# Performance work log

Measured on AMD Instinct MI355X. Metric: run time of the kernel, lower is better.

## Reference

```python
import jax, jax.numpy as jnp
import numpy as np

N_NODES = 50000
N_EDGES = 800000
N_GRAPHS = 500
NEG_SLOPE = 0.2
BN_EPS = 1e-5


def gat_layer(x, src, dst, W, al, ar, b):
    # x: [N, F_in]; W: [F_in, H*D]; al/ar: [H, D]; b: [H*D]
    H, D = al.shape
    feat = (x @ W).reshape(N_NODES, H, D)          # [N,H,D]
    el = jnp.sum(feat * al, axis=-1)               # [N,H] src-side score
    er = jnp.sum(feat * ar, axis=-1)               # [N,H] dst-side score
    e = el[src] + er[dst]                          # [E,H]
    e = jnp.where(e > 0, e, NEG_SLOPE * e)         # leaky_relu(0.2)
    # edge softmax over incoming edges of each dst node
    m = jax.ops.segment_max(e, dst, num_segments=N_NODES)       # [N,H]
    ex = jnp.exp(e - m[dst])                                    # [E,H]
    denom = jax.ops.segment_sum(ex, dst, num_segments=N_NODES)  # [N,H]
    alpha = ex / denom[dst]                                     # [E,H]
    # weighted scatter-aggregation of source features
    msg = feat[src] * alpha[:, :, None]                          # [E,H,D]
    out = jax.ops.segment_sum(msg, dst, num_segments=N_NODES)    # [N,H,D]
    return out + b.reshape(H, D)


def batch_norm(x, gamma, beta):
    # training-mode BN over node dimension (biased variance, as torch)
    mu = jnp.mean(x, axis=0)
    var = jnp.mean((x - mu) ** 2, axis=0)
    return gamma * (x - mu) * jax.lax.rsqrt(var + BN_EPS) + beta


def setup_inputs() -> dict:
    key = jax.random.key(0)
    ks = jax.random.split(key, 20)
    s = lambda shape, k, scale=0.05: jax.random.normal(ks[k], shape, jnp.float32) * scale
    return {
        "x": jax.random.normal(ks[0], (N_NODES, 128), jnp.float32),
        "edge_src": jax.random.randint(ks[1], (N_EDGES,), 0, N_NODES),
        "edge_dst": jax.random.randint(ks[2], (N_EDGES,), 0, N_NODES),
        "graph_ids": jax.random.randint(ks[3], (N_NODES,), 0, N_GRAPHS),
        "W0": s((128, 128), 4), "al0": s((4, 32), 5), "ar0": s((4, 32), 6), "b0": jnp.zeros((128,), jnp.float32),
        "W1": s((128, 128), 7), "al1": s((4, 32), 8), "ar1": s((4, 32), 9), "b1": jnp.zeros((128,), jnp.float32),
        "W2": s((128, 32), 10), "al2": s((1, 32), 11), "ar2": s((1, 32), 12), "b2": jnp.zeros((32,), jnp.float32),
        "g0": jnp.ones((128,), jnp.float32), "beta0": jnp.zeros((128,), jnp.float32),
        "g1": jnp.ones((128,), jnp.float32), "beta1": jnp.zeros((128,), jnp.float32),
        "Wc": s((32, 10), 13), "bc": jnp.zeros((10,), jnp.float32),
    }


def reference(x, edge_src, edge_dst, graph_ids,
              W0, al0, ar0, b0, W1, al1, ar1, b1, W2, al2, ar2, b2,
              g0, beta0, g1, beta1, Wc, bc):
    # layer 0: GAT -> flatten heads -> BN -> ReLU (dropout = identity in eval)
    h = gat_layer(x, edge_src, edge_dst, W0, al0, ar0, b0).reshape(N_NODES, -1)
    h = jax.nn.relu(batch_norm(h, g0, beta0))
    # layer 1
    h = gat_layer(h, edge_src, edge_dst, W1, al1, ar1, b1).reshape(N_NODES, -1)
    h = jax.nn.relu(batch_norm(h, g1, beta1))
    # layer 2 (single head) -> squeeze head dim
    h = gat_layer(h, edge_src, edge_dst, W2, al2, ar2, b2)[:, 0, :]  # [N, 32]
    # sum pooling per graph
    hg = jax.ops.segment_sum(h, graph_ids, num_segments=N_GRAPHS)    # [G, 32]
    return hg @ Wc + bc                                              # [G, 10]
```

## Files before the change

kernel.cpp:

```cpp
#include <hip/hip_runtime.h>
#include <math.h>

#define NNODES 50000
#define NEDGES 800000
#define NGRAPHS 500
#define NEG_SLOPE 0.2f
#define BN_EPS 1e-5f
#define NRANGE 196
#define RH_EPB 4096
#define RH_NB ((NEDGES + RH_EPB - 1) / RH_EPB)
#define MAXRE 5120
#define BN_NB 200
#define BN_RPB 250

typedef unsigned int uint;
typedef unsigned short ushort;
typedef __attribute__((ext_vector_type(8))) short bf16x8;
typedef __attribute__((ext_vector_type(4))) float f32x4;

__device__ __forceinline__ float bf2f(ushort u) { return __uint_as_float(((uint)u) << 16); }
__device__ __forceinline__ float bflo(uint u)   { return __uint_as_float(u << 16); }
__device__ __forceinline__ float bfhi(uint u)   { return __uint_as_float(u & 0xffff0000u); }
__device__ __forceinline__ ushort f2bf(float f) {
    uint u = __float_as_uint(f);
    u = (u + 0x7fffu + ((u >> 16) & 1u)) >> 16;
    return (ushort)u;
}

__global__ __launch_bounds__(256) void prep_hist_kernel(
        const float* __restrict__ W0, const float* __restrict__ W1,
        const float* __restrict__ W2, ushort* __restrict__ Wt0,
        ushort* __restrict__ Wt1, ushort* __restrict__ Wt2,
        const int* __restrict__ dst, int* __restrict__ rhist) {
    int t = blockIdx.x * 256 + threadIdx.x;
    if (t < 16384) {
        int k = t >> 7, m = t & 127;
        Wt0[m * 128 + k] = f2bf(W0[t]);
    } else if (t < 32768) {
        int i = t - 16384;
        int k = i >> 7, m = i & 127;
        Wt1[m * 128 + k] = f2bf(W1[i]);
    } else if (t < 36864) {
        int i = t - 32768;
        int k = i >> 5, m = i & 31;
        Wt2[m * 128 + k] = f2bf(W2[i]);
    }
    __shared__ int cnt[NRANGE];
    for (int i = threadIdx.x; i < NRANGE; i += 256) cnt[i] = 0;
    __syncthreads();
    int base = blockIdx.x * RH_EPB;
    int end = base + RH_EPB; if (end > NEDGES) end = NEDGES;
    for (int i = base + threadIdx.x; i < end; i += 256) atomicAdd(&cnt[dst[i] >> 8], 1);
    __syncthreads();
    for (int i = threadIdx.x; i < NRANGE; i += 256)
        if (cnt[i]) atomicAdd(&rhist[i], cnt[i]);
}

__global__ void range_scan_kernel(const int* __restrict__ rhist, int* __restrict__ rbase,
                                  int* __restrict__ rcursor, int* __restrict__ rowptr) {
    __shared__ int ls[256];
    int t = threadIdx.x;
    ls[t] = (t < NRANGE) ? rhist[t] : 0;
    __syncthreads();
    for (int off = 1; off < 256; off <<= 1) {
        int u = (t >= off) ? ls[t - off] : 0;
        __syncthreads();
        ls[t] += u;
        __syncthreads();
    }
    if (t < NRANGE) {
        int b = (t == 0) ? 0 : ls[t - 1];
        rbase[t] = b;
        rcursor[t] = b;
    }
    if (t == 0) { rbase[NRANGE] = NEDGES; rowptr[NNODES] = NEDGES; }
}

__global__ void reorder_kernel(const int* __restrict__ src, const int* __restrict__ dst,
                               int* __restrict__ rcursor, uint* __restrict__ bucket) {
    __shared__ int cnt[NRANGE];
    __shared__ int bofs[NRANGE];
    for (int i = threadIdx.x; i < NRANGE; i += 256) cnt[i] = 0;
    __syncthreads();
    int base = blockIdx.x * RH_EPB;
    int end = base + RH_EPB; if (end > NEDGES) end = NEDGES;
    for (int i = base + threadIdx.x; i < end; i += 256) atomicAdd(&cnt[dst[i] >> 8], 1);
    __syncthreads();
    for (int i = threadIdx.x; i < NRANGE; i += 256) {
        int c = cnt[i];
        bofs[i] = c ? atomicAdd(&rcursor[i], c) : 0;
    }
    __syncthreads();
    for (int i = threadIdx.x; i < NRANGE; i += 256) cnt[i] = 0;
    __syncthreads();
    for (int i = base + threadIdx.x; i < end; i += 256) {
        int d = dst[i], r = d >> 8;
        int loc = atomicAdd(&cnt[r], 1);
        bucket[bofs[r] + loc] = (uint)src[i] | ((uint)(d & 255) << 16);
    }
}

__global__ __launch_bounds__(256) void range_csr_kernel(const int* __restrict__ rbase,
                                                        const uint* __restrict__ bucket,
                                                        int* __restrict__ rowptr,
                                                        int* __restrict__ csr_src) {
    __shared__ uint ebuf[MAXRE];
    __shared__ int deg[256], excl[256], cur[256];
    const int r = blockIdx.x;
    const int b0 = rbase[r];
    const int cnt = rbase[r + 1] - b0;
    const int t = threadIdx.x;
    deg[t] = 0; cur[t] = 0;
    __syncthreads();
    for (int i = t; i < cnt; i += 256) {
        uint e = bucket[b0 + i];
        ebuf[i] = e;
        atomicAdd(&deg[e >> 16], 1);
    }
    __syncthreads();
    excl[t] = deg[t];
    __syncthreads();
    for (int off = 1; off < 256; off <<= 1) {
        int u = (t >= off) ? excl[t - off] : 0;
        __syncthreads();
        excl[t] += u;
        __syncthreads();
    }
    int myExcl = (t == 0) ? 0 : excl[t - 1];
    __syncthreads();
    excl[t] = myExcl;
    __syncthreads();
    int node = r * 256 + t;
    if (node < NNODES) rowptr[node] = b0 + myExcl;
    for (int i = t; i < cnt; i += 256) {
        uint e = ebuf[i];
        int dl = e >> 16;
        int loc = atomicAdd(&cur[dl], 1);
        csr_src[b0 + excl[dl] + loc] = (int)(e & 0xffffu);
    }
}

template <int M, bool HASBN>
__global__ __launch_bounds__(256) void gemm_mfma_kernel(
        const void* __restrict__ Xv, const ushort* __restrict__ Wt,
        const float* __restrict__ scale, const float* __restrict__ shift,
        const float* __restrict__ al, const float* __restrict__ ar,
        ushort* __restrict__ Y, float* __restrict__ el, float* __restrict__ er, int N) {
    constexpr int H   = M / 32;
    constexpr int BR  = (M == 128) ? 64 : 128;
    constexpr int RT  = (M == 128) ? 4 : 2;
    constexpr int CT  = 2;
    constexpr int LDK = 136;
    __shared__ ushort xs[BR][LDK];
    __shared__ ushort ws[M][LDK];
    __shared__ float scs[128], shs[128];

    const int tid = threadIdx.x, wv = tid >> 6, lane = tid & 63;
    const int rowBase = blockIdx.x * BR;

    if (HASBN) {
        if (tid < 128) {
            scs[tid] = scale[tid];
            shs[tid] = shift[tid];
        }
        __syncthreads();
    }

    if (HASBN) {
        const ushort* X = (const ushort*)Xv;
        for (int i = tid; i < BR * 16; i += 256) {
            int rr = i >> 4, q = i & 15;
            int gr = rowBase + rr;
            uint4 u = make_uint4(0, 0, 0, 0);
            if (gr < N) u = *(const uint4*)(X + (size_t)gr * 128 + q * 8);
            uint arr[4] = {u.x, u.y, u.z, u.w};
            ushort* o = &xs[rr][q * 8];
#pragma unroll
            for (int j = 0; j < 4; ++j) {
                int c = q * 8 + j * 2;
                float lo = fmaxf(bflo(arr[j]) * scs[c] + shs[c], 0.f);
                float hi = fmaxf(bfhi(arr[j]) * scs[c + 1] + shs[c + 1], 0.f);
                o[j * 2]     = f2bf(lo);
                o[j * 2 + 1] = f2bf(hi);
            }
        }
    } else {
        const float* X = (const float*)Xv;
        for (int i = tid; i < BR * 32; i += 256) {
            int rr = i >> 5, c4 = i & 31;
            int gr = rowBase + rr;
            float4 v = make_float4(0.f, 0.f, 0.f, 0.f);
            if (gr < N) v = *(const float4*)(X + (size_t)gr * 128 + c4 * 4);
            ushort* o = &xs[rr][c4 * 4];
            o[0] = f2bf(v.x); o[1] = f2bf(v.y); o[2] = f2bf(v.z); o[3] = f2bf(v.w);
        }
    }
    for (int i = tid; i < M * 16; i += 256) {
        int rr = i >> 4, kc = (i & 15) * 8;
        *(uint4*)&ws[rr][kc] = *(const uint4*)(Wt + rr * 128 + kc);
    }
    __syncthreads();

    const int waveRow = (M == 128) ? 0 : (wv * 32);
    const int waveCol = (M == 128) ? (wv * 32) : 0;
    const int fr = lane & 15, quad = lane >> 4;

    f32x4 acc[RT][CT];
#pragma unroll
    for (int rt = 0; rt < RT; ++rt)
#pragma unroll
        for (int ct = 0; ct < CT; ++ct) acc[rt][ct] = (f32x4){0.f, 0.f, 0.f, 0.f};

#pragma unroll
    for (int ks = 0; ks < 4; ++ks) {
        const int kb = ks * 32 + quad * 8;
        bf16x8 a[RT], b[CT];
#pragma unroll
        for (int rt = 0; rt < RT; ++rt) a[rt] = *(const bf16x8*)&xs[waveRow + rt * 16 + fr][kb];
#pragma unroll
        for (int ct = 0; ct < CT; ++ct) b[ct] = *(const bf16x8*)&ws[waveCol + ct * 16 + fr][kb];
#pragma unroll
        for (int rt = 0; rt < RT; ++rt)
#pragma unroll
            for (int ct = 0; ct < CT; ++ct)
                acc[rt][ct] = __builtin_amdgcn_mfma_f32_16x16x32_bf16(a[rt], b[ct], acc[rt][ct], 0, 0, 0);
    }

#pragma unroll
    for (int rt = 0; rt < RT; ++rt)
#pragma unroll
        for (int ct = 0; ct < CT; ++ct)
#pragma unroll
            for (int rg = 0; rg < 4; ++rg) {
                int gr = rowBase + waveRow + rt * 16 + quad * 4 + rg;
                int gc = waveCol + ct * 16 + fr;
                if (gr < N) Y[(size_t)gr * M + gc] = f2bf(acc[rt][ct][rg]);
            }

    const float a0 = al[waveCol + fr],      a1 = al[waveCol + 16 + fr];
    const float g0 = ar[waveCol + fr],      g1 = ar[waveCol + 16 + fr];
    const int h = (M == 128) ? wv : 0;
#pragma unroll
    for (int rt = 0; rt < RT; ++rt)
#pragma unroll
        for (int rg = 0; rg < 4; ++rg) {
            float pe = acc[rt][0][rg] * a0 + acc[rt][1][rg] * a1;
            float pr = acc[rt][0][rg] * g0 + acc[rt][1][rg] * g1;
#pragma unroll
            for (int off = 1; off < 16; off <<= 1) {
                pe += __shfl_xor(pe, off);
                pr += __shfl_xor(pr, off);
            }
            int grow = rowBase + waveRow + rt * 16 + quad * 4 + rg;
            if (fr == 0 && grow < N) {
                el[grow * H + h] = pe;
                er[grow * H + h] = pr;
            }
        }
}

__global__ __launch_bounds__(256) void gat_gather4_kernel(
        const int* __restrict__ rowptr, const int* __restrict__ csr_src,
        const float* __restrict__ el, const float* __restrict__ er,
        const ushort* __restrict__ feat, const float* __restrict__ bias,
        ushort* __restrict__ xnext) {
    const int d = __builtin_amdgcn_readfirstlane(
        (int)((blockIdx.x * blockDim.x + threadIdx.x) >> 6));
    const int lane = threadIdx.x & 63;
    if (d >= NNODES) return;
    const int h   = lane >> 4;
    const int k   = lane & 15;
    const int grp = lane & 48;
    const int c0  = lane * 2;
    const int r0 = rowptr[d];
    const int deg = rowptr[d + 1] - r0;
    const float erh = er[d * 4 + h];
    float dnm = 0.f, ax = 0.f, ay = 0.f;

    for (int j0 = 0; j0 < deg; j0 += 16) {
        int eidx = j0 + k;
        int s_e = 0;
        float ex = 0.f;
        if (eidx < deg) {
            s_e = csr_src[r0 + eidx];
            float v = el[s_e * 4 + h] + erh;
            v = v > 0.f ? v : NEG_SLOPE * v;
            ex = __expf(v);
        }
        dnm += ex;
        uint u[16];
#pragma unroll
        for (int jj = 0; jj < 16; ++jj) {
            int sj = __builtin_amdgcn_readlane(s_e, jj);
            u[jj] = *(const uint*)(feat + (size_t)sj * 128 + c0);
        }
#pragma unroll
        for (int jj = 0; jj < 16; ++jj) {
            float exj = __shfl(ex, grp + jj);
            ax = fmaf(exj, bflo(u[jj]), ax);
            ay = fmaf(exj, bfhi(u[jj]), ay);
        }
    }
#pragma unroll
    for (int off = 1; off < 16; off <<= 1) dnm += __shfl_xor(dnm, off);
    float inv = (dnm > 0.f) ? 1.f / dnm : 0.f;
    float vx = ax * inv + bias[c0];
    float vy = ay * inv + bias[c0 + 1];
    uint pk = ((uint)f2bf(vy) << 16) | (uint)f2bf(vx);
    *(uint*)(xnext + (size_t)d * 128 + c0) = pk;
}

__global__ void bn_stats_kernel(const ushort* __restrict__ X, float* __restrict__ psum,
                                float* __restrict__ psumsq) {
    const uint* X32 = (const uint*)X;
    int uc = threadIdx.x & 63;
    int rq = threadIdx.x >> 6;
    int r0 = blockIdx.x * BN_RPB;
    float s0 = 0.f, s1 = 0.f, ss0 = 0.f, ss1 = 0.f;
    for (int r = r0 + rq; r < r0 + BN_RPB; r += 4) {
        uint u = X32[(size_t)r * 64 + uc];
        float lo = bflo(u), hi = bfhi(u);
        s0 += lo; ss0 += lo * lo;
        s1 += hi; ss1 += hi * hi;
    }
    __shared__ float red[4][256], redsq[4][256];
    red[rq][uc * 2] = s0;      red[rq][uc * 2 + 1] = s1;
    redsq[rq][uc * 2] = ss0;   redsq[rq][uc * 2 + 1] = ss1;
    __syncthreads();
    int t = threadIdx.x;
    if (t < 128) {
        psum[blockIdx.x * 128 + t] = red[0][t] + red[1][t] + red[2][t] + red[3][t];
    } else {
        int c = t - 128;
        psumsq[blockIdx.x * 128 + c] = redsq[0][c] + redsq[1][c] + redsq[2][c] + redsq[3][c];
    }
}

__global__ void bn_finalize_kernel(const float* __restrict__ psum, const float* __restrict__ psumsq,
                                   const float* __restrict__ g, const float* __restrict__ beta,
                                   float* __restrict__ scale, float* __restrict__ shift) {
    int c = threadIdx.x;
    float s = 0.f, ss = 0.f;
    for (int b = 0; b < BN_NB; ++b) {
        s += psum[b * 128 + c];
        ss += psumsq[b * 128 + c];
    }
    const float inv = 1.f / NNODES;
    float mu = s * inv;
    float var = ss * inv - mu * mu;
    float sc = g[c] * rsqrtf(var + BN_EPS);
    scale[c] = sc;
    shift[c] = beta[c] - mu * sc;
}

__global__ __launch_bounds__(256) void gat_gather1_kernel(
        const int* __restrict__ rowptr, const int* __restrict__ csr_src,
        const float* __restrict__ el, const float* __restrict__ er,
        const ushort* __restrict__ feat, const float* __restrict__ bias,
        const int* __restrict__ gid, float* __restrict__ pooled) {
    const int d = __builtin_amdgcn_readfirstlane(
        (int)((blockIdx.x * blockDim.x + threadIdx.x) >> 6));
    int lane = threadIdx.x & 63;
    if (d >= NNODES) return;
    const int r0 = rowptr[d];
    const int deg = rowptr[d + 1] - r0;
    const int half = lane >> 5;
    const int c    = lane & 31;
    const float erh = er[d];
    float dnm = 0.f, acc = 0.f;

    for (int j0 = 0; j0 < deg; j0 += 32) {
        int eidx = j0 + (lane & 31);
        int s_e = 0;
        float ex = 0.f;
        if (eidx < deg) {
            s_e = csr_src[r0 + eidx];
            float v = el[s_e] + erh;
            v = v > 0.f ? v : NEG_SLOPE * v;
            ex = __expf(v);
        }
        dnm += ex;
        ushort u[16];
#pragma unroll
        for (int jj = 0; jj < 16; ++jj) {
            int sj = __shfl(s_e, 2 * jj + half);
            u[jj] = feat[(size_t)sj * 32 + c];
        }
#pragma unroll
        for (int jj = 0; jj < 16; ++jj) {
            float exj = __shfl(ex, 2 * jj + half);
            acc = fmaf(exj, bf2f(u[jj]), acc);
        }
    }
#pragma unroll
    for (int off = 1; off < 32; off <<= 1) dnm += __shfl_xor(dnm, off);
    acc += __shfl_down(acc, 32);
    if (half == 0) {
        float inv = (dnm > 0.f) ? 1.f / dnm : 0.f;
        atomicAdd(&pooled[gid[d] * 32 + c], acc * inv + bias[c]);
    }
}

__global__ void classify_kernel(const float* __restrict__ pooled, const float* __restrict__ Wc,
                                const float* __restrict__ bc, float* __restrict__ out) {
    int t = blockIdx.x * blockDim.x + threadIdx.x;
    if (t >= NGRAPHS * 10) return;
    int gIdx = t / 10, j = t % 10;
    float s = bc[j];
#pragma unroll
    for (int c = 0; c < 32; ++c) s += pooled[gIdx * 32 + c] * Wc[c * 10 + j];
    out[t] = s;
}

extern "C" void kernel_launch(void* const* d_in, const int* in_sizes, int n_in,
                              void* d_out, int out_size, void* d_ws, size_t ws_size,
                              hipStream_t stream) {
    const float* x     = (const float*)d_in[0];
    const int*   esrc  = (const int*)d_in[1];
    const int*   edst  = (const int*)d_in[2];
    const int*   gid   = (const int*)d_in[3];
    const float* W0    = (const float*)d_in[4];
    const float* al0   = (const float*)d_in[5];
    const float* ar0   = (const float*)d_in[6];
    const float* b0    = (const float*)d_in[7];
    const float* W1    = (const float*)d_in[8];
    const float* al1   = (const float*)d_in[9];
    const float* ar1   = (const float*)d_in[10];
    const float* b1    = (const float*)d_in[11];
    const float* W2    = (const float*)d_in[12];
    const float* al2   = (const float*)d_in[13];
    const float* ar2   = (const float*)d_in[14];
    const float* b2    = (const float*)d_in[15];
    const float* g0    = (const float*)d_in[16];
    const float* beta0 = (const float*)d_in[17];
    const float* g1    = (const float*)d_in[18];
    const float* beta1 = (const float*)d_in[19];
    const float* Wc    = (const float*)d_in[20];
    const float* bc    = (const float*)d_in[21];

    ushort* featbf  = (ushort*)d_ws;
    ushort* xnext   = featbf + (size_t)NNODES * 128;
    float*  el      = (float*)(xnext + (size_t)NNODES * 128);
    float*  er      = el + (size_t)NNODES * 4;
    float*  pooled  = er + (size_t)NNODES * 4;
    float*  psum    = pooled + NGRAPHS * 32;
    float*  psumsq  = psum + BN_NB * 128;
    float*  scale0  = psumsq + BN_NB * 128;
    float*  shift0  = scale0 + 128;
    float*  scale1  = shift0 + 128;
    float*  shift1  = scale1 + 128;
    int* rowptr  = (int*)(shift1 + 128);
    int* csr_src = rowptr + NNODES + 1;
    uint* bucket = (uint*)(csr_src + NEDGES);
    int* rhist   = (int*)(bucket + NEDGES);
    int* rbase   = rhist + NRANGE;
    int* rcursor = rbase + NRANGE + 1;
    ushort* Wt0  = (ushort*)(rcursor + NRANGE);
    ushort* Wt1  = Wt0 + 128 * 128;
    ushort* Wt2  = Wt1 + 128 * 128;

    const int T = 256;
    float* out = (float*)d_out;

    hipMemsetAsync(pooled, 0, (size_t)NGRAPHS * 32 * 4, stream);
    hipMemsetAsync(rhist, 0, (size_t)NRANGE * 4, stream);
    prep_hist_kernel<<<RH_NB, T, 0, stream>>>(W0, W1, W2, Wt0, Wt1, Wt2, edst, rhist);

    range_scan_kernel<<<1, T, 0, stream>>>(rhist, rbase, rcursor, rowptr);
    reorder_kernel<<<RH_NB, T, 0, stream>>>(esrc, edst, rcursor, bucket);
    range_csr_kernel<<<NRANGE, T, 0, stream>>>(rbase, bucket, rowptr, csr_src);

    const int GATHER4_BLOCKS = (NNODES * 64 + T - 1) / T;
    const int GATHER1_BLOCKS = (NNODES * 64 + T - 1) / T;
    const int GEMM128_BLOCKS = (NNODES + 63) / 64;
    const int GEMM32_BLOCKS  = (NNODES + 127) / 128;

    gemm_mfma_kernel<128, false><<<GEMM128_BLOCKS, T, 0, stream>>>(
        x, Wt0, nullptr, nullptr, al0, ar0, featbf, el, er, NNODES);
    gat_gather4_kernel<<<GATHER4_BLOCKS, T, 0, stream>>>(rowptr, csr_src, el, er, featbf, b0, xnext);
    bn_stats_kernel<<<BN_NB, T, 0, stream>>>(xnext, psum, psumsq);
    bn_finalize_kernel<<<1, 128, 0, stream>>>(psum, psumsq, g0, beta0, scale0, shift0);

    gemm_mfma_kernel<128, true><<<GEMM128_BLOCKS, T, 0, stream>>>(
        xnext, Wt1, scale0, shift0, al1, ar1, featbf, el, er, NNODES);
    gat_gather4_kernel<<<GATHER4_BLOCKS, T, 0, stream>>>(rowptr, csr_src, el, er, featbf, b1, xnext);
    bn_stats_kernel<<<BN_NB, T, 0, stream>>>(xnext, psum, psumsq);
    bn_finalize_kernel<<<1, 128, 0, stream>>>(psum, psumsq, g1, beta1, scale1, shift1);

    gemm_mfma_kernel<32, true><<<GEMM32_BLOCKS, T, 0, stream>>>(
        xnext, Wt2, scale1, shift1, al2, ar2, featbf, el, er, NNODES);
    gat_gather1_kernel<<<GATHER1_BLOCKS, T, 0, stream>>>(rowptr, csr_src, el, er, featbf, b2,
                                                         gid, pooled);

    classify_kernel<<<(NGRAPHS * 10 + T - 1) / T, T, 0, stream>>>(pooled, Wc, bc, out);
}
```

Measured before the change: 352.4 us.

## Cut kernel launches by fusing scan, BN finalize and classifier into neighbours

New measurement: 607.1 us. 1.72x slower.

```diff
diff --git a/kernel.cpp b/kernel.cpp
--- a/kernel.cpp
+++ b/kernel.cpp
@@ -27,12 +27,21 @@
     return (ushort)u;
 }
 
+__device__ __forceinline__ float ld_dev(const float* p) {
+    return __hip_atomic_load(p, __ATOMIC_RELAXED, __HIP_MEMORY_SCOPE_AGENT);
+}
+__device__ __forceinline__ void st_dev(float* p, float v) {
+    __hip_atomic_store(p, v, __ATOMIC_RELAXED, __HIP_MEMORY_SCOPE_AGENT);
+}
+
 __global__ __launch_bounds__(256) void prep_hist_kernel(
         const float* __restrict__ W0, const float* __restrict__ W1,
         const float* __restrict__ W2, ushort* __restrict__ Wt0,
         ushort* __restrict__ Wt1, ushort* __restrict__ Wt2,
-        const int* __restrict__ dst, int* __restrict__ rhist) {
+        const int* __restrict__ dst, int* __restrict__ rhist,
+        int* __restrict__ rowptr) {
     int t = blockIdx.x * 256 + threadIdx.x;
+    if (t == 0) rowptr[NNODES] = NEDGES;
     if (t < 16384) {
         int k = t >> 7, m = t & 127;
         Wt0[m * 128 + k] = f2bf(W0[t]);
@@ -56,60 +65,62 @@
         if (cnt[i]) atomicAdd(&rhist[i], cnt[i]);
 }
 
-__global__ void range_scan_kernel(const int* __restrict__ rhist, int* __restrict__ rbase,
-                                  int* __restrict__ rcursor, int* __restrict__ rowptr) {
-    __shared__ int ls[256];
-    int t = threadIdx.x;
-    ls[t] = (t < NRANGE) ? rhist[t] : 0;
-    __syncthreads();
-    for (int off = 1; off < 256; off <<= 1) {
-        int u = (t >= off) ? ls[t - off] : 0;
-        __syncthreads();
-        ls[t] += u;
-        __syncthreads();
-    }
-    if (t < NRANGE) {
-        int b = (t == 0) ? 0 : ls[t - 1];
-        rbase[t] = b;
-        rcursor[t] = b;
-    }
-    if (t == 0) { rbase[NRANGE] = NEDGES; rowptr[NNODES] = NEDGES; }
-}
-
-__global__ void reorder_kernel(const int* __restrict__ src, const int* __restrict__ dst,
-                               int* __restrict__ rcursor, uint* __restrict__ bucket) {
+__global__ __launch_bounds__(256) void reorder_kernel(
+        const int* __restrict__ src, const int* __restrict__ dst,
+        const int* __restrict__ rhist, int* __restrict__ rcursor,
+        uint* __restrict__ bucket) {
     __shared__ int cnt[NRANGE];
     __shared__ int bofs[NRANGE];
-    for (int i = threadIdx.x; i < NRANGE; i += 256) cnt[i] = 0;
-    __syncthreads();
+    __shared__ int rb[256];
+    const int t = threadIdx.x;
+    rb[t] = (t < NRANGE) ? rhist[t] : 0;
+    cnt[t < NRANGE ? t : 0] = 0;
+    if (t < NRANGE) cnt[t] = 0;
+    __syncthreads();
+    for (int off = 1; off < 256; off <<= 1) {
+        int u = (t >= off) ? rb[t - off] : 0;
+        __syncthreads();
+        rb[t] += u;
+        __syncthreads();
+    }
     int base = blockIdx.x * RH_EPB;
     int end = base + RH_EPB; if (end > NEDGES) end = NEDGES;
-    for (int i = base + threadIdx.x; i < end; i += 256) atomicAdd(&cnt[dst[i] >> 8], 1);
-    __syncthreads();
-    for (int i = threadIdx.x; i < NRANGE; i += 256) {
+    for (int i = base + t; i < end; i += 256) atomicAdd(&cnt[dst[i] >> 8], 1);
+    __syncthreads();
+    for (int i = t; i < NRANGE; i += 256) {
         int c = cnt[i];
-        bofs[i] = c ? atomicAdd(&rcursor[i], c) : 0;
-    }
-    __syncthreads();
-    for (int i = threadIdx.x; i < NRANGE; i += 256) cnt[i] = 0;
-    __syncthreads();
-    for (int i = base + threadIdx.x; i < end; i += 256) {
+        int ex = (i == 0) ? 0 : rb[i - 1];
+        bofs[i] = c ? (ex + atomicAdd(&rcursor[i], c)) : 0;
+    }
+    __syncthreads();
+    for (int i = t; i < NRANGE; i += 256) cnt[i] = 0;
+    __syncthreads();
+    for (int i = base + t; i < end; i += 256) {
         int d = dst[i], r = d >> 8;
         int loc = atomicAdd(&cnt[r], 1);
         bucket[bofs[r] + loc] = (uint)src[i] | ((uint)(d & 255) << 16);
     }
 }
 
-__global__ __launch_bounds__(256) void range_csr_kernel(const int* __restrict__ rbase,
+__global__ __launch_bounds__(256) void range_csr_kernel(const int* __restrict__ rhist,
                                                         const uint* __restrict__ bucket,
                                                         int* __restrict__ rowptr,
                                                         int* __restrict__ csr_src) {
     __shared__ uint ebuf[MAXRE];
     __shared__ int deg[256], excl[256], cur[256];
+    __shared__ int rb[256];
     const int r = blockIdx.x;
-    const int b0 = rbase[r];
-    const int cnt = rbase[r + 1] - b0;
     const int t = threadIdx.x;
+    rb[t] = (t < NRANGE) ? rhist[t] : 0;
+    __syncthreads();
+    for (int off = 1; off < 256; off <<= 1) {
+        int u = (t >= off) ? rb[t - off] : 0;
+        __syncthreads();
+        rb[t] += u;
+        __syncthreads();
+    }
+    const int b0 = (r == 0) ? 0 : rb[r - 1];
+    const int cnt = rb[r] - b0;
     deg[t] = 0; cur[t] = 0;
     __syncthreads();
     for (int i = t; i < cnt; i += 256) {
@@ -310,8 +321,10 @@
     *(uint*)(xnext + (size_t)d * 128 + c0) = pk;
 }
 
-__global__ void bn_stats_kernel(const ushort* __restrict__ X, float* __restrict__ psum,
-                                float* __restrict__ psumsq) {
+__global__ __launch_bounds__(256) void bn_stats_kernel(
+        const ushort* __restrict__ X, float* __restrict__ psum, float* __restrict__ psumsq,
+        const float* __restrict__ g, const float* __restrict__ beta,
+        float* __restrict__ scale, float* __restrict__ shift, int* __restrict__ counter) {
     const uint* X32 = (const uint*)X;
     int uc = threadIdx.x & 63;
     int rq = threadIdx.x >> 6;
@@ -329,39 +342,45 @@
     __syncthreads();
     int t = threadIdx.x;
     if (t < 128) {
-        psum[blockIdx.x * 128 + t] = red[0][t] + red[1][t] + red[2][t] + red[3][t];
+        st_dev(&psum[blockIdx.x * 128 + t], red[0][t] + red[1][t] + red[2][t] + red[3][t]);
     } else {
         int c = t - 128;
-        psumsq[blockIdx.x * 128 + c] = redsq[0][c] + redsq[1][c] + redsq[2][c] + redsq[3][c];
-    }
-}
-
-__global__ void bn_finalize_kernel(const float* __restrict__ psum, const float* __restrict__ psumsq,
-                                   const float* __restrict__ g, const float* __restrict__ beta,
-                                   float* __restrict__ scale, float* __restrict__ shift) {
-    int c = threadIdx.x;
-    float s = 0.f, ss = 0.f;
-    for (int b = 0; b < BN_NB; ++b) {
-        s += psum[b * 128 + c];
-        ss += psumsq[b * 128 + c];
-    }
-    const float inv = 1.f / NNODES;
-    float mu = s * inv;
-    float var = ss * inv - mu * mu;
-    float sc = g[c] * rsqrtf(var + BN_EPS);
-    scale[c] = sc;
-    shift[c] = beta[c] - mu * sc;
+        st_dev(&psumsq[blockIdx.x * 128 + c], redsq[0][c] + redsq[1][c] + redsq[2][c] + redsq[3][c]);
+    }
+    __syncthreads();
+    __shared__ int isLast;
+    if (t == 0) {
+        __threadfence();
+        isLast = (atomicAdd(counter, 1) == (int)gridDim.x - 1);
+    }
+    __syncthreads();
+    if (!isLast) return;
+    __threadfence();
+    if (t < 128) {
+        float s = 0.f, ss = 0.f;
+        for (int b = 0; b < BN_NB; ++b) {
+            s += ld_dev(&psum[b * 128 + t]);
+            ss += ld_dev(&psumsq[b * 128 + t]);
+        }
+        const float inv = 1.f / NNODES;
+        float mu = s * inv;
+        float var = ss * inv - mu * mu;
+        float sc = g[t] * rsqrtf(var + BN_EPS);
+        scale[t] = sc;
+        shift[t] = beta[t] - mu * sc;
+    }
 }
 
 __global__ __launch_bounds__(256) void gat_gather1_kernel(
         const int* __restrict__ rowptr, const int* __restrict__ csr_src,
         const float* __restrict__ el, const float* __restrict__ er,
         const ushort* __restrict__ feat, const float* __restrict__ bias,
-        const int* __restrict__ gid, float* __restrict__ pooled) {
+        const int* __restrict__ gid, float* __restrict__ pooled,
+        const float* __restrict__ Wc, const float* __restrict__ bc,
+        float* __restrict__ out, int* __restrict__ counter) {
     const int d = __builtin_amdgcn_readfirstlane(
         (int)((blockIdx.x * blockDim.x + threadIdx.x) >> 6));
     int lane = threadIdx.x & 63;
-    if (d >= NNODES) return;
     const int r0 = rowptr[d];
     const int deg = rowptr[d + 1] - r0;
     const int half = lane >> 5;
@@ -399,17 +418,27 @@
         float inv = (dnm > 0.f) ? 1.f / dnm : 0.f;
         atomicAdd(&pooled[gid[d] * 32 + c], acc * inv + bias[c]);
     }
-}
-
-__global__ void classify_kernel(const float* __restrict__ pooled, const float* __restrict__ Wc,
-                                const float* __restrict__ bc, float* __restrict__ out) {
-    int t = blockIdx.x * blockDim.x + threadIdx.x;
-    if (t >= NGRAPHS * 10) return;
-    int gIdx = t / 10, j = t % 10;
-    float s = bc[j];
-#pragma unroll
-    for (int c = 0; c < 32; ++c) s += pooled[gIdx * 32 + c] * Wc[c * 10 + j];
-    out[t] = s;
+    __syncthreads();
+    __shared__ int isLast;
+    if (threadIdx.x == 0) {
+        __threadfence();
+        isLast = (atomicAdd(counter, 1) == (int)gridDim.x - 1);
+    }
+    __syncthreads();
+    if (!isLast) return;
+    __threadfence();
+    for (int g = threadIdx.x; g < NGRAPHS; g += 256) {
+        float pv[32];
+#pragma unroll
+        for (int cc = 0; cc < 32; ++cc) pv[cc] = ld_dev(&pooled[g * 32 + cc]);
+#pragma unroll
+        for (int j = 0; j < 10; ++j) {
+            float s = bc[j];
+#pragma unroll
+            for (int cc = 0; cc < 32; ++cc) s = fmaf(pv[cc], Wc[cc * 10 + j], s);
+            out[g * 10 + j] = s;
+        }
+    }
 }
 
 extern "C" void kernel_launch(void* const* d_in, const int* in_sizes, int n_in,
@@ -438,59 +467,56 @@
     const float* Wc    = (const float*)d_in[20];
     const float* bc    = (const float*)d_in[21];
 
-    ushort* featbf  = (ushort*)d_ws;
-    ushort* xnext   = featbf + (size_t)NNODES * 128;
-    float*  el      = (float*)(xnext + (size_t)NNODES * 128);
-    float*  er      = el + (size_t)NNODES * 4;
-    float*  pooled  = er + (size_t)NNODES * 4;
-    float*  psum    = pooled + NGRAPHS * 32;
-    float*  psumsq  = psum + BN_NB * 128;
-    float*  scale0  = psumsq + BN_NB * 128;
-    float*  shift0  = scale0 + 128;
-    float*  scale1  = shift0 + 128;
-    float*  shift1  = scale1 + 128;
-    int* rowptr  = (int*)(shift1 + 128);
-    int* csr_src = rowptr + NNODES + 1;
-    uint* bucket = (uint*)(csr_src + NEDGES);
-    int* rhist   = (int*)(bucket + NEDGES);
-    int* rbase   = rhist + NRANGE;
-    int* rcursor = rbase + NRANGE + 1;
-    ushort* Wt0  = (ushort*)(rcursor + NRANGE);
-    ushort* Wt1  = Wt0 + 128 * 128;
-    ushort* Wt2  = Wt1 + 128 * 128;
+    int*   counters = (int*)d_ws;
+    int*   rhist    = counters + 8;
+    int*   rcursor  = rhist + NRANGE;
+    float* pooled   = (float*)(rcursor + NRANGE);
+    float* psum     = pooled + NGRAPHS * 32;
+    float* psumsq   = psum + BN_NB * 128;
+    float* scale0   = psumsq + BN_NB * 128;
+    float* shift0   = scale0 + 128;
+    float* scale1   = shift0 + 128;
+    float* shift1   = scale1 + 128;
+    int*   rowptr   = (int*)(shift1 + 128);
+    int*   csr_src  = rowptr + NNODES + 1;
+    uint*  bucket   = (uint*)(csr_src + NEDGES);
+    size_t ofs = (size_t)((int*)(bucket + NEDGES) - (int*)d_ws);
+    ofs = (ofs + 3) & ~(size_t)3;
+    ushort* featbf = (ushort*)((int*)d_ws + ofs);
+    ushort* xnext  = featbf + (size_t)NNODES * 128;
+    float*  el     = (float*)(xnext + (size_t)NNODES * 128);
+    float*  er     = el + (size_t)NNODES * 4;
+    ushort* Wt0    = (ushort*)(er + (size_t)NNODES * 4);
+    ushort* Wt1    = Wt0 + 128 * 128;
+    ushort* Wt2    = Wt1 + 128 * 128;
 
     const int T = 256;
     float* out = (float*)d_out;
 
-    hipMemsetAsync(pooled, 0, (size_t)NGRAPHS * 32 * 4, stream);
-    hipMemsetAsync(rhist, 0, (size_t)NRANGE * 4, stream);
-    prep_hist_kernel<<<RH_NB, T, 0, stream>>>(W0, W1, W2, Wt0, Wt1, Wt2, edst, rhist);
-
-    range_scan_kernel<<<1, T, 0, stream>>>(rhist, rbase, rcursor, rowptr);
-    reorder_kernel<<<RH_NB, T, 0, stream>>>(esrc, edst, rcursor, bucket);
-    range_csr_kernel<<<NRANGE, T, 0, stream>>>(rbase, bucket, rowptr, csr_src);
-
-    const int GATHER4_BLOCKS = (NNODES * 64 + T - 1) / T;
-    const int GATHER1_BLOCKS = (NNODES * 64 + T - 1) / T;
+    hipMemsetAsync(counters, 0, (size_t)(8 + NRANGE + NRANGE + NGRAPHS * 32) * 4, stream);
+    prep_hist_kernel<<<RH_NB, T, 0, stream>>>(W0, W1, W2, Wt0, Wt1, Wt2, edst, rhist, rowptr);
+
+    reorder_kernel<<<RH_NB, T, 0, stream>>>(esrc, edst, rhist, rcursor, bucket);
+    range_csr_kernel<<<NRANGE, T, 0, stream>>>(rhist, bucket, rowptr, csr_src);
+
+    const int GATHER_BLOCKS  = (NNODES * 64) / T;
     const int GEMM128_BLOCKS = (NNODES + 63) / 64;
     const int GEMM32_BLOCKS  = (NNODES + 127) / 128;
 
     gemm_mfma_kernel<128, false><<<GEMM128_BLOCKS, T, 0, stream>>>(
         x, Wt0, nullptr, nullptr, al0, ar0, featbf, el, er, NNODES);
-    gat_gather4_kernel<<<GATHER4_BLOCKS, T, 0, stream>>>(rowptr, csr_src, el, er, featbf, b0, xnext);
-    bn_stats_kernel<<<BN_NB, T, 0, stream>>>(xnext, psum, psumsq);
-    bn_finalize_kernel<<<1, 128, 0, stream>>>(psum, psumsq, g0, beta0, scale0, shift0);
+    gat_gather4_kernel<<<GATHER_BLOCKS, T, 0, stream>>>(rowptr, csr_src, el, er, featbf, b0, xnext);
+    bn_stats_kernel<<<BN_NB, T, 0, stream>>>(xnext, psum, psumsq, g0, beta0, scale0, shift0,
+                                             &counters[0]);
 
     gemm_mfma_kernel<128, true><<<GEMM128_BLOCKS, T, 0, stream>>>(
         xnext, Wt1, scale0, shift0, al1, ar1, featbf, el, er, NNODES);
-    gat_gather4_kernel<<<GATHER4_BLOCKS, T, 0, stream>>>(rowptr, csr_src, el, er, featbf, b1, xnext);
-    bn_stats_kernel<<<BN_NB, T, 0, stream>>>(xnext, psum, psumsq);
-    bn_finalize_kernel<<<1, 128, 0, stream>>>(psum, psumsq, g1, beta1, scale1, shift1);
+    gat_gather4_kernel<<<GATHER_BLOCKS, T, 0, stream>>>(rowptr, csr_src, el, er, featbf, b1, xnext);
+    bn_stats_kernel<<<BN_NB, T, 0, stream>>>(xnext, psum, psumsq, g1, beta1, scale1, shift1,
+                                             &counters[1]);
 
     gemm_mfma_kernel<32, true><<<GEMM32_BLOCKS, T, 0, stream>>>(
         xnext, Wt2, scale1, shift1, al2, ar2, featbf, el, er, NNODES);
-    gat_gather1_kernel<<<GATHER1_BLOCKS, T, 0, stream>>>(rowptr, csr_src, el, er, featbf, b2,
-                                                         gid, pooled);
-
-    classify_kernel<<<(NGRAPHS * 10 + T - 1) / T, T, 0, stream>>>(pooled, Wc, bc, out);
-}
+    gat_gather1_kernel<<<GATHER_BLOCKS, T, 0, stream>>>(rowptr, csr_src, el, er, featbf, b2,
+                                                        gid, pooled, Wc, bc, out, &counters[2]);
+}
```
